# Performance work log

Hardware: AMD Instinct MI355X
Metric: run time of the kernel (lower is better)

## Reference

```python
import jax, jax.numpy as jnp
import numpy as np

DIM = 1024
N_HEADS = 16
D_HEAD = DIM // N_HEADS


def setup_inputs() -> dict:
    key = jax.random.key(0)
    ks = jax.random.split(key, 7)
    s = DIM ** -0.5
    return {
        "x": jax.random.normal(ks[0], (4, 2048, DIM), dtype=jnp.float32),
        "Wq": jax.random.normal(ks[1], (DIM, DIM), dtype=jnp.float32) * s,
        "bq": jax.random.normal(ks[2], (DIM,), dtype=jnp.float32) * 0.02,
        "Wk": jax.random.normal(ks[3], (DIM, DIM), dtype=jnp.float32) * s,
        "bk": jax.random.normal(ks[4], (DIM,), dtype=jnp.float32) * 0.02,
        "Wv": jax.random.normal(ks[5], (DIM, DIM), dtype=jnp.float32) * s,
        "bv": jax.random.normal(ks[6], (DIM,), dtype=jnp.float32) * 0.02,
    }


def reference(x, Wq, bq, Wk, bk, Wv, bv):
    B, N, D = x.shape
    H, Dh = N_HEADS, D_HEAD

    def split_heads(t):
        # b n (h d) -> b h n d
        return t.reshape(B, N, H, Dh).transpose(0, 2, 1, 3)

    q = split_heads(x @ Wq + bq)
    k = split_heads(x @ Wk + bk)
    v = split_heads(x @ Wv + bv)

    scale = Dh ** -0.5
    logit = jnp.einsum("bhnd,bhmd->bhnm", q, k) * scale  # [B,H,N,N]
    attn = jax.nn.softmax(logit, axis=-1)
    out = jnp.einsum("bhnm,bhmd->bhnd", attn, v)
    # b h n d -> b n (h d)
    return out.transpose(0, 2, 1, 3).reshape(B, N, D)
```

## Files before the change

### kernel.cpp

```cpp
#include <hip/hip_runtime.h>
#include <hip/hip_bf16.h>
#include <stdint.h>

#define BB 4
#define SEQ 2048
#define DIM 1024
#define NH 16
#define DH 64
#define MM (BB*SEQ)

typedef unsigned short u16;
typedef __attribute__((ext_vector_type(8))) __bf16 bf16x8;
typedef __attribute__((ext_vector_type(4))) float floatx4;
typedef __attribute__((ext_vector_type(16))) float floatx16;
typedef __attribute__((ext_vector_type(2))) float floatx2;
typedef __attribute__((ext_vector_type(4))) unsigned short u16x4;
typedef __attribute__((ext_vector_type(2))) unsigned int uint2v;

#define QSCALE 0.18033688011112042f

__device__ __forceinline__ u16 f2bf(float f) {
    union { float f; unsigned u; } v; v.f = f;
    unsigned u = v.u;
    u += 0x7FFF + ((u >> 16) & 1);
    return (u16)(u >> 16);
}

__device__ __forceinline__ bf16x8 ldb8(const u16* p) {
    return *(const bf16x8*)(const void*)p;
}

__device__ __forceinline__ void async_copy16(const u16* g, u16* l) {
    __builtin_amdgcn_global_load_lds(
        (const __attribute__((address_space(1))) unsigned int*)g,
        (__attribute__((address_space(3))) unsigned int*)l, 16, 0, 0);
}

__device__ __forceinline__ floatx16 mfma32(bf16x8 a, bf16x8 b, floatx16 c) {
    return __builtin_amdgcn_mfma_f32_32x32x16_bf16(a, b, c, 0, 0, 0);
}

__device__ __forceinline__ unsigned cvtpk(float lo, float hi) {
    unsigned r;
    asm("v_cvt_pk_bf16_f32 %0, %1, %2" : "=v"(r) : "v"(lo), "v"(hi));
    return r;
}

__global__ __launch_bounds__(256)
void prep(const float* __restrict__ x, u16* __restrict__ xb,
          const float* __restrict__ Wq, const float* __restrict__ Wk,
          const float* __restrict__ Wv, u16* __restrict__ Wt) {
    const int bx = blockIdx.x;
    const int tid = threadIdx.x;
    if (bx < 8192) {
        const size_t i = ((size_t)bx * 256 + tid) * 4;
        float4 f = *(const float4*)(x + i);
        u16x4 o = { f2bf(f.x), f2bf(f.y), f2bf(f.z), f2bf(f.w) };
        *(u16x4*)(xb + i) = o;
        return;
    }
    const int idx = bx - 8192;
    const int t = idx >> 8;
    const int r2 = idx & 255;
    const int k0 = (r2 >> 4) * 64, n0 = (r2 & 15) * 64;
    const float* W = (t == 0) ? Wq : (t == 1) ? Wk : Wv;
    u16* D = Wt + (size_t)t * DIM * DIM;
    __shared__ u16 T[64][65];
    #pragma unroll
    for (int p = 0; p < 4; p++) {
        const int r = p * 16 + (tid >> 4), c = (tid & 15) * 4;
        float4 f = *(const float4*)(W + (size_t)(k0 + r) * DIM + n0 + c);
        T[c + 0][r] = f2bf(f.x); T[c + 1][r] = f2bf(f.y);
        T[c + 2][r] = f2bf(f.z); T[c + 3][r] = f2bf(f.w);
    }
    __syncthreads();
    #pragma unroll
    for (int p = 0; p < 4; p++) {
        const int rn = p * 16 + (tid >> 4), ck = (tid & 15) * 4;
        u16x4 v = { T[rn][ck], T[rn][ck + 1], T[rn][ck + 2], T[rn][ck + 3] };
        *(u16x4*)(D + (size_t)(n0 + rn) * DIM + k0 + ck) = v;
    }
}

__global__ __launch_bounds__(256, 3)
void qkv_gemm3(const u16* __restrict__ xb, const u16* __restrict__ Wt,
               const float* __restrict__ bq, const float* __restrict__ bk,
               const float* __restrict__ bv, u16* __restrict__ ws) {
    __shared__ u16 As[2][4096];
    __shared__ u16 Bs[2][4096];

    const int m0 = blockIdx.x * 128;
    const int t  = blockIdx.y >> 3;
    const int c0 = (blockIdx.y & 7) * 128;
    const u16* Wtb = Wt + (size_t)t * DIM * DIM;
    const float* bias = (t == 0) ? bq : (t == 1) ? bk : bv;
    const float osc = (t == 0) ? QSCALE : 1.0f;
    u16* dst = ws + (size_t)t * ((size_t)MM * DIM);

    const int tid  = threadIdx.x;
    const int lane = tid & 63;
    const int w    = tid >> 6;
    const int wr = w >> 1, wc = w & 1;
    const int g = lane >> 4, ln = lane & 15;

    floatx4 acc[4][4];
    #pragma unroll
    for (int i = 0; i < 4; i++)
        #pragma unroll
        for (int j = 0; j < 4; j++) acc[i][j] = (floatx4){0.f,0.f,0.f,0.f};

    const int srow = w*16 + (lane >> 2);
    const int gseg = (lane & 3) ^ ((lane >> 3) & 3);
    const u16* gA = xb  + (size_t)(m0 + srow) * DIM + gseg*8;
    const u16* gB = Wtb + (size_t)(c0 + srow) * DIM + gseg*8;

    async_copy16(gA,                   &As[0][w*512]);
    async_copy16(gA + (size_t)64*DIM,  &As[0][2048 + w*512]);
    async_copy16(gB,                   &Bs[0][w*512]);
    async_copy16(gB + (size_t)64*DIM,  &Bs[0][2048 + w*512]);
    __syncthreads();

    const int xu = (ln >> 1) & 3;

    for (int it = 0; it < 32; it++) {
        const int cur = it & 1;
        if (it < 31) {
            const int nxt = cur ^ 1;
            const int kk = (it + 1) * 32;
            async_copy16(gA + kk,                  &As[nxt][w*512]);
            async_copy16(gA + kk + (size_t)64*DIM, &As[nxt][2048 + w*512]);
            async_copy16(gB + kk,                  &Bs[nxt][w*512]);
            async_copy16(gB + kk + (size_t)64*DIM, &Bs[nxt][2048 + w*512]);
        }

        bf16x8 a[4], b[4];
        #pragma unroll
        for (int fr = 0; fr < 4; fr++)
            a[fr] = ldb8(&As[cur][(wr*64 + fr*16 + ln)*32 + (g ^ xu)*8]);
        #pragma unroll
        for (int fc = 0; fc < 4; fc++)
            b[fc] = ldb8(&Bs[cur][(wc*64 + fc*16 + ln)*32 + (g ^ xu)*8]);

        if (t < 2) {
            #pragma unroll
            for (int fr = 0; fr < 4; fr++)
                #pragma unroll
                for (int fc = 0; fc < 4; fc++)
                    acc[fr][fc] = __builtin_amdgcn_mfma_f32_16x16x32_bf16(
                        b[fc], a[fr], acc[fr][fc], 0, 0, 0);
        } else {
            #pragma unroll
            for (int fr = 0; fr < 4; fr++)
                #pragma unroll
                for (int fc = 0; fc < 4; fc++)
                    acc[fr][fc] = __builtin_amdgcn_mfma_f32_16x16x32_bf16(
                        a[fr], b[fc], acc[fr][fc], 0, 0, 0);
        }
        __syncthreads();
    }

    if (t < 2) {
        #pragma unroll
        for (int fc = 0; fc < 4; fc++) {
            const int cc = c0 + wc*64 + fc*16 + g*4;
            const float4 b4 = *(const float4*)&bias[cc];
            const int h = cc >> 6, d = cc & 63;
            #pragma unroll
            for (int fr = 0; fr < 4; fr++) {
                const int tok = m0 + wr*64 + fr*16 + ln;
                const int bidx = tok >> 11, nn = tok & 2047;
                u16x4 v = { f2bf((acc[fr][fc][0] + b4.x) * osc),
                            f2bf((acc[fr][fc][1] + b4.y) * osc),
                            f2bf((acc[fr][fc][2] + b4.z) * osc),
                            f2bf((acc[fr][fc][3] + b4.w) * osc) };
                *(u16x4*)&dst[((size_t)(bidx*NH + h)*SEQ + nn)*DH + d] = v;
            }
        }
    } else {
        #pragma unroll
        for (int fc = 0; fc < 4; fc++) {
            const int cc = c0 + wc*64 + fc*16 + ln;
            const float bias_v = bias[cc];
            const int h = cc >> 6, d = cc & 63;
            #pragma unroll
            for (int fr = 0; fr < 4; fr++) {
                const int mrow = m0 + wr*64 + fr*16 + g*4;
                const int bidx = mrow >> 11, nn = mrow & 2047;
                u16x4 v = { f2bf(acc[fr][fc][0] + bias_v), f2bf(acc[fr][fc][1] + bias_v),
                            f2bf(acc[fr][fc][2] + bias_v), f2bf(acc[fr][fc][3] + bias_v) };
                *(u16x4*)&dst[((size_t)(bidx*NH + h)*DH + d)*SEQ + nn] = v;
            }
        }
    }
}

#define LDA 40
__global__ __launch_bounds__(256)
void qkv_gemm(const float* __restrict__ x,
              const float* __restrict__ Wq, const float* __restrict__ bq,
              const float* __restrict__ Wk, const float* __restrict__ bk,
              const float* __restrict__ Wv, const float* __restrict__ bv,
              u16* __restrict__ ws) {
    __shared__ u16 As[128 * LDA];
    __shared__ u16 Bs[128 * LDA];
    const int m0 = blockIdx.x * 128;
    const int t  = blockIdx.y >> 3;
    const int c0 = (blockIdx.y & 7) * 128;
    const float* W    = (t == 0) ? Wq : (t == 1) ? Wk : Wv;
    const float* bias = (t == 0) ? bq : (t == 1) ? bk : bv;
    const float osc = (t == 0) ? QSCALE : 1.0f;
    u16* dst = ws + (size_t)t * ((size_t)MM * DIM);
    const int tid  = threadIdx.x;
    const int lane = tid & 63;
    const int wave = tid >> 6;
    const int wr = wave >> 1, wc = wave & 1;
    const int g = lane >> 4, ln = lane & 15;
    floatx4 acc[4][4];
    #pragma unroll
    for (int i = 0; i < 4; i++)
        #pragma unroll
        for (int j = 0; j < 4; j++) acc[i][j] = (floatx4){0.f,0.f,0.f,0.f};
    const int ar  = tid >> 1;
    const int ak  = (tid & 1) * 16;
    const int bkr = tid & 31;
    const int bc  = (tid >> 5) * 16;
    for (int kk = 0; kk < DIM; kk += 32) {
        {
            const float4* s4 = (const float4*)(x + (size_t)(m0 + ar) * DIM + kk + ak);
            float4 f0 = s4[0], f1 = s4[1], f2 = s4[2], f3 = s4[3];
            unsigned pk[8];
            pk[0] = f2bf(f0.x) | ((unsigned)f2bf(f0.y) << 16);
            pk[1] = f2bf(f0.z) | ((unsigned)f2bf(f0.w) << 16);
            pk[2] = f2bf(f1.x) | ((unsigned)f2bf(f1.y) << 16);
            pk[3] = f2bf(f1.z) | ((unsigned)f2bf(f1.w) << 16);
            pk[4] = f2bf(f2.x) | ((unsigned)f2bf(f2.y) << 16);
            pk[5] = f2bf(f2.z) | ((unsigned)f2bf(f2.w) << 16);
            pk[6] = f2bf(f3.x) | ((unsigned)f2bf(f3.y) << 16);
            pk[7] = f2bf(f3.z) | ((unsigned)f2bf(f3.w) << 16);
            uint4* d = (uint4*)&As[ar * LDA + ak];
            d[0] = make_uint4(pk[0], pk[1], pk[2], pk[3]);
            d[1] = make_uint4(pk[4], pk[5], pk[6], pk[7]);
        }
        {
            const float4* s4 = (const float4*)(W + (size_t)(kk + bkr) * DIM + c0 + bc);
            float4 f0 = s4[0], f1 = s4[1], f2 = s4[2], f3 = s4[3];
            float fv[16] = {f0.x,f0.y,f0.z,f0.w, f1.x,f1.y,f1.z,f1.w,
                            f2.x,f2.y,f2.z,f2.w, f3.x,f3.y,f3.z,f3.w};
            #pragma unroll
            for (int j = 0; j < 16; j++)
                Bs[(bc + j) * LDA + bkr] = f2bf(fv[j]);
        }
        __syncthreads();
        bf16x8 a[4], b[4];
        #pragma unroll
        for (int fr = 0; fr < 4; fr++)
            a[fr] = ldb8(&As[(wr*64 + fr*16 + ln) * LDA + g*8]);
        #pragma unroll
        for (int fc = 0; fc < 4; fc++)
            b[fc] = ldb8(&Bs[(wc*64 + fc*16 + ln) * LDA + g*8]);
        #pragma unroll
        for (int fr = 0; fr < 4; fr++)
            #pragma unroll
            for (int fc = 0; fc < 4; fc++)
                acc[fr][fc] = __builtin_amdgcn_mfma_f32_16x16x32_bf16(
                    a[fr], b[fc], acc[fr][fc], 0, 0, 0);
        __syncthreads();
    }
    #pragma unroll
    for (int fc = 0; fc < 4; fc++) {
        const int cc = c0 + wc*64 + fc*16 + ln;
        const float bias_v = bias[cc];
        const int h = cc >> 6, d = cc & 63;
        #pragma unroll
        for (int fr = 0; fr < 4; fr++) {
            #pragma unroll
            for (int rr = 0; rr < 4; rr++) {
                const int mrow = m0 + wr*64 + fr*16 + g*4 + rr;
                const int bidx = mrow >> 11, nn = mrow & 2047;
                const float val = (acc[fr][fc][rr] + bias_v) * osc;
                size_t idx;
                if (t < 2) idx = ((size_t)(bidx*NH + h)*SEQ + nn)*DH + d;
                else       idx = ((size_t)(bidx*NH + h)*DH + d)*SEQ + nn;
                dst[idx] = f2bf(val);
            }
        }
    }
}

__global__ __launch_bounds__(256, 2)
void attn11(const u16* __restrict__ ws, float* __restrict__ out) {
    const int bid = blockIdx.x;
    const int qt = bid >> 6;
    const int bh = bid & 63;
    const int b  = bh >> 4;
    const int h  = bh & 15;

    const u16* Qw = ws;
    const u16* Kw = ws + (size_t)MM * DIM;
    const u16* Vt = ws + 2 * (size_t)MM * DIM;

    __shared__ u16 Kbuf[4][4096];
    __shared__ u16 Vbuf[4][4096];

    const int tid  = threadIdx.x;
    const int lane = tid & 63;
    const int w    = tid >> 6;
    const int l31  = lane & 31;
    const int hi   = lane >> 5;
    const int c7   = lane & 7;
    const int q0w  = qt*256 + w*64;

    const int srow = w*16 + (lane >> 3);
    const int sseg = (lane & 7) ^ ((lane >> 3) & 7);
    const u16* kg = Kw + ((size_t)bh*SEQ + srow)*DH + sseg*8;
    const u16* vg = Vt + ((size_t)bh*DH + srow)*SEQ + sseg*8;

    bf16x8 qf[2][4];
    #pragma unroll
    for (int qs = 0; qs < 2; qs++) {
        const u16* qp = Qw + ((size_t)bh*SEQ + q0w + qs*32 + l31)*DH + hi*8;
        #pragma unroll
        for (int ds = 0; ds < 4; ds++) qf[qs][ds] = ldb8(qp + ds*16);
    }

    floatx16 accO[2][2];
    #pragma unroll
    for (int qs = 0; qs < 2; qs++)
        #pragma unroll
        for (int fd = 0; fd < 2; fd++)
            #pragma unroll
            for (int r = 0; r < 16; r++) accO[qs][fd][r] = 0.f;
    floatx2 lr2[2] = { (floatx2){0.f,0.f}, (floatx2){0.f,0.f} };
    floatx16 fz;
    #pragma unroll
    for (int r = 0; r < 16; r++) fz[r] = 0.f;

    #pragma unroll
    for (int t = 0; t < 3; t++) {
        async_copy16(kg + (size_t)t*64*DH,           &Kbuf[t][w*1024]);
        async_copy16(kg + (size_t)t*64*DH + 8*DH,    &Kbuf[t][w*1024 + 512]);
        async_copy16(vg + (size_t)t*64,              &Vbuf[t][w*1024]);
        async_copy16(vg + (size_t)t*64 + (size_t)8*SEQ, &Vbuf[t][w*1024 + 512]);
    }

    for (int kt = 0; kt < 32; kt++) {
        if (kt < 30)       asm volatile("s_waitcnt vmcnt(8)" ::: "memory");
        else if (kt == 30) asm volatile("s_waitcnt vmcnt(4)" ::: "memory");
        else               asm volatile("s_waitcnt vmcnt(0)" ::: "memory");
        __builtin_amdgcn_s_barrier();
        __builtin_amdgcn_sched_barrier(0);

        if (kt < 29) {
            const int t3 = kt + 3;
            async_copy16(kg + (size_t)t3*64*DH,           &Kbuf[t3 & 3][w*1024]);
            async_copy16(kg + (size_t)t3*64*DH + 8*DH,    &Kbuf[t3 & 3][w*1024 + 512]);
            async_copy16(vg + (size_t)t3*64,              &Vbuf[t3 & 3][w*1024]);
            async_copy16(vg + (size_t)t3*64 + (size_t)8*SEQ, &Vbuf[t3 & 3][w*1024 + 512]);
        }

        const u16* Kc = &Kbuf[kt & 3][0];
        const u16* Vc = &Vbuf[kt & 3][0];

        #pragma unroll
        for (int kb = 0; kb < 2; kb++) {
            const u16* krow = &Kc[(kb*32 + l31)*64];
            bf16x8 kf0 = ldb8(&krow[((0 + hi) ^ c7)*8]);
            bf16x8 kf1 = ldb8(&krow[((2 + hi) ^ c7)*8]);
            bf16x8 kf2 = ldb8(&krow[((4 + hi) ^ c7)*8]);
            bf16x8 kf3 = ldb8(&krow[((6 + hi) ^ c7)*8]);

            floatx16 z0 = mfma32(kf0, qf[0][0], fz);
            floatx16 z1 = mfma32(kf0, qf[1][0], fz);
            z0 = mfma32(kf1, qf[0][1], z0);
            z1 = mfma32(kf1, qf[1][1], z1);
            z0 = mfma32(kf2, qf[0][2], z0);
            z1 = mfma32(kf2, qf[1][2], z1);
            z0 = mfma32(kf3, qf[0][3], z0);
            z1 = mfma32(kf3, qf[1][3], z1);

            union { unsigned u[4]; bf16x8 v; } bpA0, bpA1, bpB0, bpB1;
            {
                float p[16];
                #pragma unroll
                for (int r = 0; r < 16; r++) p[r] = __builtin_amdgcn_exp2f(z0[r]);
                #pragma unroll
                for (int i = 0; i < 8; i++) lr2[0] += (floatx2){p[2*i], p[2*i+1]};
                unsigned c[8];
                #pragma unroll
                for (int i = 0; i < 8; i++) c[i] = cvtpk(p[2*i], p[2*i+1]);
                uint2v s02 = __builtin_amdgcn_permlane32_swap(c[0], c[2], false, false);
                uint2v s13 = __builtin_amdgcn_permlane32_swap(c[1], c[3], false, false);
                uint2v s46 = __builtin_amdgcn_permlane32_swap(c[4], c[6], false, false);
                uint2v s57 = __builtin_amdgcn_permlane32_swap(c[5], c[7], false, false);
                bpA0.u[0] = s02[0]; bpA0.u[1] = s13[0]; bpA0.u[2] = s02[1]; bpA0.u[3] = s13[1];
                bpA1.u[0] = s46[0]; bpA1.u[1] = s57[0]; bpA1.u[2] = s46[1]; bpA1.u[3] = s57[1];
            }
            {
                float p[16];
                #pragma unroll
                for (int r = 0; r < 16; r++) p[r] = __builtin_amdgcn_exp2f(z1[r]);
                #pragma unroll
                for (int i = 0; i < 8; i++) lr2[1] += (floatx2){p[2*i], p[2*i+1]};
                unsigned c[8];
                #pragma unroll
                for (int i = 0; i < 8; i++) c[i] = cvtpk(p[2*i], p[2*i+1]);
                uint2v s02 = __builtin_amdgcn_permlane32_swap(c[0], c[2], false, false);
                uint2v s13 = __builtin_amdgcn_permlane32_swap(c[1], c[3], false, false);
                uint2v s46 = __builtin_amdgcn_permlane32_swap(c[4], c[6], false, false);
                uint2v s57 = __builtin_amdgcn_permlane32_swap(c[5], c[7], false, false);
                bpB0.u[0] = s02[0]; bpB0.u[1] = s13[0]; bpB0.u[2] = s02[1]; bpB0.u[3] = s13[1];
                bpB1.u[0] = s46[0]; bpB1.u[1] = s57[0]; bpB1.u[2] = s46[1]; bpB1.u[3] = s57[1];
            }

            bf16x8 av00 = ldb8(&Vc[(0*32 + l31)*64 + ((kb*4 + 0 + hi) ^ c7)*8]);
            bf16x8 av01 = ldb8(&Vc[(0*32 + l31)*64 + ((kb*4 + 2 + hi) ^ c7)*8]);
            bf16x8 av10 = ldb8(&Vc[(1*32 + l31)*64 + ((kb*4 + 0 + hi) ^ c7)*8]);
            bf16x8 av11 = ldb8(&Vc[(1*32 + l31)*64 + ((kb*4 + 2 + hi) ^ c7)*8]);
            accO[0][0] = mfma32(av00, bpA0.v, accO[0][0]);
            accO[1][0] = mfma32(av00, bpB0.v, accO[1][0]);
            accO[0][1] = mfma32(av10, bpA0.v, accO[0][1]);
            accO[1][1] = mfma32(av10, bpB0.v, accO[1][1]);
            accO[0][0] = mfma32(av01, bpA1.v, accO[0][0]);
            accO[1][0] = mfma32(av01, bpB1.v, accO[1][0]);
            accO[0][1] = mfma32(av11, bpA1.v, accO[0][1]);
            accO[1][1] = mfma32(av11, bpB1.v, accO[1][1]);
        }
    }

    #pragma unroll
    for (int qs = 0; qs < 2; qs++) {
        float v = lr2[qs][0] + lr2[qs][1];
        v += __shfl_xor(v, 32, 64);
        const float inv = 1.0f / v;
        const int n = q0w + qs*32 + l31;
        float* orow = &out[((size_t)b*SEQ + n)*DIM + h*DH];
        #pragma unroll
        for (int fd = 0; fd < 2; fd++)
            #pragma unroll
            for (int rp = 0; rp < 4; rp++) {
                const int d = fd*32 + rp*8 + hi*4;
                float4 o = { accO[qs][fd][rp*4+0]*inv, accO[qs][fd][rp*4+1]*inv,
                             accO[qs][fd][rp*4+2]*inv, accO[qs][fd][rp*4+3]*inv };
                *(float4*)&orow[d] = o;
            }
    }
}

extern "C" void kernel_launch(void* const* d_in, const int* in_sizes, int n_in,
                              void* d_out, int out_size, void* d_ws, size_t ws_size,
                              hipStream_t stream) {
    const float* x  = (const float*)d_in[0];
    const float* Wq = (const float*)d_in[1];
    const float* bq = (const float*)d_in[2];
    const float* Wk = (const float*)d_in[3];
    const float* bk = (const float*)d_in[4];
    const float* Wv = (const float*)d_in[5];
    const float* bv = (const float*)d_in[6];
    u16* ws = (u16*)d_ws;
    float* out = (float*)d_out;

    const size_t need = (size_t)4 * MM * DIM * 2 + (size_t)3 * DIM * DIM * 2;
    if (ws_size >= need) {
        u16* xb = ws + (size_t)3 * MM * DIM;
        u16* Wt = ws + (size_t)4 * MM * DIM;
        prep<<<dim3(8192 + 768), 256, 0, stream>>>(x, xb, Wq, Wk, Wv, Wt);
        qkv_gemm3<<<dim3(MM/128, 24), 256, 0, stream>>>(xb, Wt, bq, bk, bv, ws);
    } else {
        qkv_gemm<<<dim3(MM/128, 24), 256, 0, stream>>>(x, Wq, bq, Wk, bk, Wv, bv, ws);
    }
    attn11<<<dim3((SEQ/256) * NH * BB), 256, 0, stream>>>(ws, out);
}
```

Measured before the change: 250.4 us.

## Merge Q/K/V GEMM blocks so three warp groups share one x tile

The QKV projection kernel now launches 768-thread blocks. Three 4-wave groups each compute one of Q, K or V for the same 128x128 output tile, sharing a single double-buffered A (x) tile in LDS. This removes the redundant loading of x tiles, which were previously fetched separately by each of the three projections. In exchange, LDS per block grows, blocks become larger, and the 6-blocks launch bound may constrain registers or occupancy.

```diff
diff --git a/kernel.cpp b/kernel.cpp
--- a/kernel.cpp
+++ b/kernel.cpp
@@ -82,42 +82,46 @@
     }
 }
 
-__global__ __launch_bounds__(256, 3)
-void qkv_gemm3(const u16* __restrict__ xb, const u16* __restrict__ Wt,
-               const float* __restrict__ bq, const float* __restrict__ bk,
-               const float* __restrict__ bv, u16* __restrict__ ws) {
+__global__ __launch_bounds__(768, 6)
+void qkv_gemm3m(const u16* __restrict__ xb, const u16* __restrict__ Wt,
+                const float* __restrict__ bq, const float* __restrict__ bk,
+                const float* __restrict__ bv, u16* __restrict__ ws) {
     __shared__ u16 As[2][4096];
-    __shared__ u16 Bs[2][4096];
+    __shared__ u16 Bs[3][2][4096];
 
     const int m0 = blockIdx.x * 128;
-    const int t  = blockIdx.y >> 3;
-    const int c0 = (blockIdx.y & 7) * 128;
-    const u16* Wtb = Wt + (size_t)t * DIM * DIM;
-    const float* bias = (t == 0) ? bq : (t == 1) ? bk : bv;
-    const float osc = (t == 0) ? QSCALE : 1.0f;
-    u16* dst = ws + (size_t)t * ((size_t)MM * DIM);
+    const int c0 = blockIdx.y * 128;
 
     const int tid  = threadIdx.x;
     const int lane = tid & 63;
     const int w    = tid >> 6;
-    const int wr = w >> 1, wc = w & 1;
+    const int tg   = w >> 2;
+    const int wl   = w & 3;
+    const int wr = wl >> 1, wc = wl & 1;
     const int g = lane >> 4, ln = lane & 15;
 
+    const u16* Wtb = Wt + (size_t)tg * DIM * DIM;
+    const float* bias = (tg == 0) ? bq : (tg == 1) ? bk : bv;
+    const float osc = (tg == 0) ? QSCALE : 1.0f;
+    u16* dst = ws + (size_t)tg * ((size_t)MM * DIM);
+
     floatx4 acc[4][4];
     #pragma unroll
     for (int i = 0; i < 4; i++)
         #pragma unroll
         for (int j = 0; j < 4; j++) acc[i][j] = (floatx4){0.f,0.f,0.f,0.f};
 
-    const int srow = w*16 + (lane >> 2);
+    const int srow = wl*16 + (lane >> 2);
     const int gseg = (lane & 3) ^ ((lane >> 3) & 3);
     const u16* gA = xb  + (size_t)(m0 + srow) * DIM + gseg*8;
     const u16* gB = Wtb + (size_t)(c0 + srow) * DIM + gseg*8;
 
-    async_copy16(gA,                   &As[0][w*512]);
-    async_copy16(gA + (size_t)64*DIM,  &As[0][2048 + w*512]);
-    async_copy16(gB,                   &Bs[0][w*512]);
-    async_copy16(gB + (size_t)64*DIM,  &Bs[0][2048 + w*512]);
+    if (tg == 0) {
+        async_copy16(gA,                  &As[0][wl*512]);
+        async_copy16(gA + (size_t)64*DIM, &As[0][2048 + wl*512]);
+    }
+    async_copy16(gB,                  &Bs[tg][0][wl*512]);
+    async_copy16(gB + (size_t)64*DIM, &Bs[tg][0][2048 + wl*512]);
     __syncthreads();
 
     const int xu = (ln >> 1) & 3;
@@ -127,10 +131,12 @@
         if (it < 31) {
             const int nxt = cur ^ 1;
             const int kk = (it + 1) * 32;
-            async_copy16(gA + kk,                  &As[nxt][w*512]);
-            async_copy16(gA + kk + (size_t)64*DIM, &As[nxt][2048 + w*512]);
-            async_copy16(gB + kk,                  &Bs[nxt][w*512]);
-            async_copy16(gB + kk + (size_t)64*DIM, &Bs[nxt][2048 + w*512]);
+            if (tg == 0) {
+                async_copy16(gA + kk,                  &As[nxt][wl*512]);
+                async_copy16(gA + kk + (size_t)64*DIM, &As[nxt][2048 + wl*512]);
+            }
+            async_copy16(gB + kk,                  &Bs[tg][nxt][wl*512]);
+            async_copy16(gB + kk + (size_t)64*DIM, &Bs[tg][nxt][2048 + wl*512]);
         }
 
         bf16x8 a[4], b[4];
@@ -139,9 +145,9 @@
             a[fr] = ldb8(&As[cur][(wr*64 + fr*16 + ln)*32 + (g ^ xu)*8]);
         #pragma unroll
         for (int fc = 0; fc < 4; fc++)
-            b[fc] = ldb8(&Bs[cur][(wc*64 + fc*16 + ln)*32 + (g ^ xu)*8]);
-
-        if (t < 2) {
+            b[fc] = ldb8(&Bs[tg][cur][(wc*64 + fc*16 + ln)*32 + (g ^ xu)*8]);
+
+        if (tg < 2) {
             #pragma unroll
             for (int fr = 0; fr < 4; fr++)
                 #pragma unroll
@@ -159,7 +165,7 @@
         __syncthreads();
     }
 
-    if (t < 2) {
+    if (tg < 2) {
         #pragma unroll
         for (int fc = 0; fc < 4; fc++) {
             const int cc = c0 + wc*64 + fc*16 + g*4;
@@ -464,7 +470,7 @@
         u16* xb = ws + (size_t)3 * MM * DIM;
         u16* Wt = ws + (size_t)4 * MM * DIM;
         prep<<<dim3(8192 + 768), 256, 0, stream>>>(x, xb, Wq, Wk, Wv, Wt);
-        qkv_gemm3<<<dim3(MM/128, 24), 256, 0, stream>>>(xb, Wt, bq, bk, bv, ws);
+        qkv_gemm3m<<<dim3(MM/128, 8), 768, 0, stream>>>(xb, Wt, bq, bk, bv, ws);
     } else {
         qkv_gemm<<<dim3(MM/128, 24), 256, 0, stream>>>(x, Wq, bq, Wk, bk, Wv, bv, ws);
     }
```

New measurement: 527.9 us. 111% more time.
